# Kernel tuning notes

Measured on AMD Instinct MI355X. Metric: run time of the kernel, lower is better.

Reference implementation:

```python
import jax, jax.numpy as jnp
import numpy as np

B, N, D, H = 4, 2048, 256, 4
DH = D // H
LN_EPS = 1e-5


def setup_inputs() -> dict:
    key = jax.random.key(0)
    ks = jax.random.split(key, 8)
    x = jax.random.normal(ks[0], (B, N, D), dtype=jnp.float32)
    adj = jax.random.randint(ks[1], (N, N), 0, 2, dtype=jnp.int32)
    # parameters (PyTorch Linear stores W as [out, in]; we store [out,in] and apply x @ W.T)
    W = jax.random.normal(ks[2], (D, D), dtype=jnp.float32) * (1.0 / np.sqrt(D))
    a_src = jax.random.normal(ks[3], (H, DH), dtype=jnp.float32)
    a_dst = jax.random.normal(ks[4], (H, DH), dtype=jnp.float32)
    Wo = jax.random.normal(ks[5], (D, D), dtype=jnp.float32) * (1.0 / np.sqrt(D))
    bo = jnp.zeros((D,), dtype=jnp.float32)
    gamma = jnp.ones((D,), dtype=jnp.float32)
    beta = jnp.zeros((D,), dtype=jnp.float32)
    return {"x": x, "adj": adj, "W": W, "a_src": a_src, "a_dst": a_dst,
            "Wo": Wo, "bo": bo, "gamma": gamma, "beta": beta}


def _layer_norm(y, gamma, beta):
    mu = jnp.mean(y, axis=-1, keepdims=True)
    var = jnp.mean((y - mu) ** 2, axis=-1, keepdims=True)
    return (y - mu) * jax.lax.rsqrt(var + LN_EPS) * gamma + beta


def reference(x, adj, W, a_src, a_dst, Wo, bo, gamma, beta):
    # dropout in eval mode (identity)
    b, n, d = x.shape
    h = (x @ W.T).reshape(b, n, H, DH).transpose(0, 2, 1, 3)  # [B,H,N,DH]
    src = jnp.einsum('bhnd,hd->bhn', h, a_src)  # [B,H,N]
    dst = jnp.einsum('bhnd,hd->bhn', h, a_dst)  # [B,H,N]
    e = src[:, :, :, None] + dst[:, :, None, :]  # e[b,h,i,j] = src_i + dst_j
    e = jnp.where(e >= 0, e, 0.2 * e)  # leaky_relu(0.2)
    mask = (adj > 0)[None, None, :, :]
    e = jnp.where(mask, e, -jnp.inf)
    attn = jax.nn.softmax(e, axis=-1)  # [B,H,N,N]
    out = jnp.einsum('bhij,bhjd->bhid', attn, h)  # [B,H,N,DH]
    out = out.transpose(0, 2, 1, 3).reshape(b, n, d)
    out = out @ Wo.T + bo
    return _layer_norm(x + out, gamma, beta)
```

## Files before the change

### kernel.cpp

```cpp
#include <hip/hip_runtime.h>
#include <stdint.h>

#define NTOK 2048
#define DMODEL 256
#define NHEAD 4

typedef __attribute__((ext_vector_type(8))) short short8;
typedef __attribute__((ext_vector_type(4))) float f32x4;

#define MFMA16(a, b, c) __builtin_amdgcn_mfma_f32_16x16x32_bf16(a, b, c, 0, 0, 0)

#if __has_builtin(__builtin_amdgcn_exp2f)
#define EXP2(x) __builtin_amdgcn_exp2f(x)
#else
#define EXP2(x) __expf((x) * 0.6931471805599453f)
#endif

__device__ __forceinline__ unsigned short f2bf(float f) {
  union { float f; unsigned int u; } v; v.f = f;
  unsigned int r = v.u + 0x7FFFu + ((v.u >> 16) & 1u);
  return (unsigned short)(r >> 16);
}

__device__ __forceinline__ f32x4 zero4() {
  f32x4 v; v[0] = 0.f; v[1] = 0.f; v[2] = 0.f; v[3] = 0.f; return v;
}

__global__ void k_prep_pack(const float* __restrict__ x, const float* __restrict__ W,
                            const float* __restrict__ Wo, const int* __restrict__ adj,
                            unsigned short* __restrict__ xbf, unsigned short* __restrict__ Wbf,
                            unsigned short* __restrict__ Wobf,
                            unsigned long long* __restrict__ bits) {
  const int b = blockIdx.x;
  if (b < 2176) {
    int e = (b * 256 + threadIdx.x) * 4;
    const float* s; unsigned short* d; int off;
    if (e < 2097152)              { s = x;  d = xbf;  off = e; }
    else if (e < 2097152 + 65536) { s = W;  d = Wbf;  off = e - 2097152; }
    else                          { s = Wo; d = Wobf; off = e - 2162688; }
    float4 v = *(const float4*)(s + off);
    ushort4 o;
    o.x = f2bf(v.x); o.y = f2bf(v.y); o.z = f2bf(v.z); o.w = f2bf(v.w);
    *(ushort4*)(d + off) = o;
  } else {
    int g = (b - 2176) * 256 + threadIdx.x;
    int v = adj[g];
    unsigned long long m = __ballot(v > 0);
    if ((threadIdx.x & 63) == 0) bits[g >> 6] = m;
  }
}

__global__ void k_gemm1(const unsigned short* __restrict__ xbf, const unsigned short* __restrict__ Wbf,
                        const float* __restrict__ a_src, const float* __restrict__ a_dst,
                        unsigned short* __restrict__ hTg, float* __restrict__ srcv,
                        float* __restrict__ dstv) {
  __shared__ float tile[64][65];
  __shared__ float reds[2][4][64];
  const int tid = threadIdx.x, lane = tid & 63, w = tid >> 6;
  const int g0 = blockIdx.x * 64;
  const int hh = blockIdx.y;
  const int n0 = hh * 64;
  const int l15 = lane & 15, kl = (lane >> 4) * 8;

  const unsigned short* arow = xbf + (size_t)(g0 + w * 16 + l15) * 256 + kl;
  const unsigned short* brow = Wbf + (size_t)(n0 + l15) * 256 + kl;

  f32x4 acc[4];
#pragma unroll
  for (int nf = 0; nf < 4; ++nf) acc[nf] = zero4();

#pragma unroll
  for (int k = 0; k < 256; k += 32) {
    short8 a = *(const short8*)(arow + k);
#pragma unroll
    for (int nf = 0; nf < 4; ++nf) {
      short8 b = *(const short8*)(brow + nf * 4096 + k);
      acc[nf] = MFMA16(a, b, acc[nf]);
    }
  }

  const int rbase = w * 16 + (lane >> 4) * 4;
#pragma unroll
  for (int nf = 0; nf < 4; ++nf)
#pragma unroll
    for (int r = 0; r < 4; ++r)
      tile[rbase + r][nf * 16 + l15] = acc[nf][r];
  __syncthreads();

  const int bh = (g0 >> 11) * NHEAD + hh;
  {
    const int dh = tid >> 2, nq = (tid & 3) * 16;
    const int c = ((g0 & 2047) + nq) >> 5;
    const int k0 = (nq & 16) >> 3;
    unsigned short* dp = hTg + (size_t)bh * 131072 + c * 2048 + dh * 32 + k0 * 8;
    short8 v0, v1;
#pragma unroll
    for (int q = 0; q < 8; ++q) v0[q] = (short)f2bf(tile[nq + q][dh]);
#pragma unroll
    for (int q = 0; q < 8; ++q) v1[q] = (short)f2bf(tile[nq + 8 + q][dh]);
    *(short8*)dp = v0;
    *(short8*)(dp + 8) = v1;
  }
  {
    const int n_loc = tid & 63, q4 = tid >> 6;
    const float* as = a_src + hh * 64 + q4 * 16;
    const float* ad = a_dst + hh * 64 + q4 * 16;
    float ps = 0.f, pd = 0.f;
#pragma unroll
    for (int d2 = 0; d2 < 16; ++d2) {
      float hv = tile[n_loc][q4 * 16 + d2];
      ps += hv * as[d2];
      pd += hv * ad[d2];
    }
    reds[0][q4][n_loc] = ps;
    reds[1][q4][n_loc] = pd;
  }
  __syncthreads();
  if (tid < 64) {
    float s = reds[0][0][tid] + reds[0][1][tid] + reds[0][2][tid] + reds[0][3][tid];
    float d = reds[1][0][tid] + reds[1][1][tid] + reds[1][2][tid] + reds[1][3][tid];
    srcv[(size_t)bh * 2048 + (g0 & 2047) + tid] = s;
    dstv[(size_t)bh * 2048 + (g0 & 2047) + tid] = d;
  }
}

__global__ __launch_bounds__(512, 4) void k_attn(
    const unsigned short* __restrict__ hTg, const float* __restrict__ srcv,
    const float* __restrict__ dstv, const unsigned long long* __restrict__ bits,
    unsigned short* __restrict__ attb) {
  __shared__ float bB_s[2048];
  __shared__ float dD_s[2048];
  __shared__ unsigned long long adjw[64][33];
  __shared__ float src_s[64];
  __shared__ float red[8];
  __shared__ float comb[2][64][40];

  const int tid = threadIdx.x, lane = tid & 63, w = tid >> 6;
  const int orig = blockIdx.x;
  const int lid = (orig & 7) * 64 + (orig >> 3);
  const int bh = lid >> 5;
  const int i0 = (lid & 31) * 64;
  const int rg = w & 1, js = w >> 1;
  const float LOG2E = 1.4426950408889634f;

  float lmax = -3.0e38f;
  {
    const float* dsrc = dstv + (size_t)bh * 2048;
    int idx = tid * 4;
    float4 v = *(const float4*)(dsrc + idx);
    v.x *= LOG2E; v.y *= LOG2E; v.z *= LOG2E; v.w *= LOG2E;
    lmax = fmaxf(fmaxf(v.x, v.y), fmaxf(v.z, v.w));
    float4 Bv, Dv;
    Bv.x = EXP2(v.x); Bv.y = EXP2(v.y); Bv.z = EXP2(v.z); Bv.w = EXP2(v.w);
    Dv.x = EXP2(0.2f * v.x); Dv.y = EXP2(0.2f * v.y);
    Dv.z = EXP2(0.2f * v.z); Dv.w = EXP2(0.2f * v.w);
    *(float4*)(bB_s + idx) = Bv;
    *(float4*)(dD_s + idx) = Dv;
#pragma unroll
    for (int off = 32; off >= 1; off >>= 1) lmax = fmaxf(lmax, __shfl_xor(lmax, off));
    if (lane == 0) red[w] = lmax;
    if (tid < 64) src_s[tid] = srcv[(size_t)bh * 2048 + i0 + tid] * LOG2E;
#pragma unroll
    for (int t = 0; t < 4; ++t) {
      int q = tid + t * 512;
      adjw[q >> 5][q & 31] = bits[(size_t)(i0 + (q >> 5)) * 32 + (q & 31)];
    }
  }
  __syncthreads();
  const float dmax = fmaxf(fmaxf(fmaxf(red[0], red[1]), fmaxf(red[2], red[3])),
                           fmaxf(fmaxf(red[4], red[5]), fmaxf(red[6], red[7])));

  const int l15 = lane & 15, klg = lane >> 4, kl = klg * 8;
  const float src0 = src_s[rg * 32 + l15];
  const float src1 = src_s[rg * 32 + 16 + l15];
  const float sa0 = src0 + dmax, sa1 = src1 + dmax;
  const float m0 = fmaxf(sa0, 0.2f * sa0);
  const float m1 = fmaxf(sa1, 0.2f * sa1);
  const float A0 = EXP2(src0 - m0), C0 = EXP2(fmaf(0.2f, src0, -m0));
  const float A1 = EXP2(src1 - m1), C1 = EXP2(fmaf(0.2f, src1, -m1));
  const float thB0 = EXP2(fminf(fmaxf(-src0, -125.f), 125.f));
  const float thB1 = EXP2(fminf(fmaxf(-src1, -125.f), 125.f));
  const int il0 = rg * 32 + l15, il1 = il0 + 16;
  const int wsel = js >> 1, wsh = (js & 1) * 32 + kl;

  const unsigned short* hgb = hTg + (size_t)bh * 131072;
  const int fragoff = l15 * 32 + klg * 8;

  short8 ones;
#pragma unroll
  for (int q = 0; q < 8; ++q) ones[q] = (short)0x3F80;

  f32x4 acc[2][4], accs[2];
#pragma unroll
  for (int rh = 0; rh < 2; ++rh) {
    accs[rh] = zero4();
#pragma unroll
    for (int nf = 0; nf < 4; ++nf) acc[rh][nf] = zero4();
  }

  short8 pA0, pA1, pA2, pA3, pB0, pB1, pB2, pB3;
  {
    const unsigned short* kp = hgb + js * 2048 + fragoff;
    pA0 = *(const short8*)(kp);
    pA1 = *(const short8*)(kp + 512);
    pA2 = *(const short8*)(kp + 1024);
    pA3 = *(const short8*)(kp + 1536);
  }

#define GAT_TILE(T, C0_, C1_, C2_, C3_, N0_, N1_, N2_, N3_)                       \
  {                                                                               \
    if ((T) < 15) {                                                               \
      const unsigned short* kp = hgb + (((T) + 1) * 4 + js) * 2048 + fragoff;     \
      N0_ = *(const short8*)(kp);                                                 \
      N1_ = *(const short8*)(kp + 512);                                           \
      N2_ = *(const short8*)(kp + 1024);                                          \
      N3_ = *(const short8*)(kp + 1536);                                          \
    }                                                                             \
    const int jo = (T) * 128 + js * 32 + kl;                                      \
    float4 b0 = *(const float4*)(bB_s + jo);                                      \
    float4 b1 = *(const float4*)(bB_s + jo + 4);                                  \
    float4 e0 = *(const float4*)(dD_s + jo);                                      \
    float4 e1 = *(const float4*)(dD_s + jo + 4);                                  \
    float bv[8] = {b0.x, b0.y, b0.z, b0.w, b1.x, b1.y, b1.z, b1.w};               \
    float dq[8] = {e0.x, e0.y, e0.z, e0.w, e1.x, e1.y, e1.z, e1.w};               \
    const unsigned long long w0_ = adjw[il0][2 * (T) + wsel];                     \
    const unsigned long long w1_ = adjw[il1][2 * (T) + wsel];                     \
    {                                                                             \
      const unsigned int byte = (unsigned int)(w0_ >> wsh) & 0xFFu;               \
      float p[8];                                                                 \
      _Pragma("unroll") for (int t8 = 0; t8 < 8; ++t8) {                          \
        const bool pos = bv[t8] >= thB0;                                          \
        const float pv = (pos ? A0 : C0) * (pos ? bv[t8] : dq[t8]);               \
        p[t8] = ((byte >> t8) & 1u) ? pv : 0.f;                                   \
      }                                                                           \
      union { short8 s8; unsigned int u32[4]; } af;                               \
      _Pragma("unroll") for (int q = 0; q < 4; ++q)                               \
        asm("v_cvt_pk_bf16_f32 %0, %1, %2"                                       \
            : "=v"(af.u32[q]) : "v"(p[2 * q]), "v"(p[2 * q + 1]));                \
      accs[0] = MFMA16(af.s8, ones, accs[0]);                                     \
      acc[0][0] = MFMA16(af.s8, C0_, acc[0][0]);                                  \
      acc[0][1] = MFMA16(af.s8, C1_, acc[0][1]);                                  \
      acc[0][2] = MFMA16(af.s8, C2_, acc[0][2]);                                  \
      acc[0][3] = MFMA16(af.s8, C3_, acc[0][3]);                                  \
    }                                                                             \
    {                                                                             \
      const unsigned int byte = (unsigned int)(w1_ >> wsh) & 0xFFu;               \
      float p[8];                                                                 \
      _Pragma("unroll") for (int t8 = 0; t8 < 8; ++t8) {                          \
        const bool pos = bv[t8] >= thB1;                                          \
        const float pv = (pos ? A1 : C1) * (pos ? bv[t8] : dq[t8]);               \
        p[t8] = ((byte >> t8) & 1u) ? pv : 0.f;                                   \
      }                                                                           \
      union { short8 s8; unsigned int u32[4]; } af;                               \
      _Pragma("unroll") for (int q = 0; q < 4; ++q)                               \
        asm("v_cvt_pk_bf16_f32 %0, %1, %2"                                       \
            : "=v"(af.u32[q]) : "v"(p[2 * q]), "v"(p[2 * q + 1]));                \
      accs[1] = MFMA16(af.s8, ones, accs[1]);                                     \
      acc[1][0] = MFMA16(af.s8, C0_, acc[1][0]);                                  \
      acc[1][1] = MFMA16(af.s8, C1_, acc[1][1]);                                  \
      acc[1][2] = MFMA16(af.s8, C2_, acc[1][2]);                                  \
      acc[1][3] = MFMA16(af.s8, C3_, acc[1][3]);                                  \
    }                                                                             \
  }

#pragma unroll 1
  for (int tt = 0; tt < 16; tt += 2) {
    GAT_TILE(tt, pA0, pA1, pA2, pA3, pB0, pB1, pB2, pB3);
    GAT_TILE(tt + 1, pB0, pB1, pB2, pB3, pA0, pA1, pA2, pA3);
  }
#undef GAT_TILE

#pragma unroll 1
  for (int s = 1; s < 4; ++s) {
    if (js == s) {
#pragma unroll
      for (int rh = 0; rh < 2; ++rh) {
#pragma unroll
        for (int nf = 0; nf < 4; ++nf)
#pragma unroll
          for (int r = 0; r < 4; ++r) comb[rg][lane][rh * 20 + nf * 4 + r] = acc[rh][nf][r];
#pragma unroll
        for (int r = 0; r < 4; ++r) comb[rg][lane][rh * 20 + 16 + r] = accs[rh][r];
      }
    }
    __syncthreads();
    if (js == 0) {
#pragma unroll
      for (int rh = 0; rh < 2; ++rh) {
#pragma unroll
        for (int nf = 0; nf < 4; ++nf)
#pragma unroll
          for (int r = 0; r < 4; ++r) acc[rh][nf][r] += comb[rg][lane][rh * 20 + nf * 4 + r];
#pragma unroll
        for (int r = 0; r < 4; ++r) accs[rh][r] += comb[rg][lane][rh * 20 + 16 + r];
      }
    }
    __syncthreads();
  }

  if (js == 0) {
    const int rb = klg * 4;
    const int b = bh >> 2, hh2 = bh & 3;
#pragma unroll
    for (int rh = 0; rh < 2; ++rh) {
      float linv[4];
#pragma unroll
      for (int r = 0; r < 4; ++r) linv[r] = 1.f / accs[rh][r];
#pragma unroll
      for (int nf = 0; nf < 4; ++nf)
#pragma unroll
        for (int r = 0; r < 4; ++r) {
          int i = i0 + rg * 32 + rh * 16 + rb + r;
          size_t o = ((size_t)(b * 2048 + i)) * 256 + hh2 * 64 + nf * 16 + l15;
          attb[o] = f2bf(acc[rh][nf][r] * linv[r]);
        }
    }
  }
}

__global__ void k_gemm2(const unsigned short* __restrict__ attb, const unsigned short* __restrict__ Wobf,
                        const float* __restrict__ bo, const float* __restrict__ x,
                        const float* __restrict__ gamma, const float* __restrict__ beta,
                        float* __restrict__ out) {
  __shared__ float tile[32][260];
  const int tid = threadIdx.x, lane = tid & 63, w = tid >> 6;
  const int g0 = blockIdx.x * 32;
  const int l15 = lane & 15, kl = (lane >> 4) * 8;
  const int rw = (w & 1) * 16;
  const int cb = (w >> 1) * 128;

  const unsigned short* arow = attb + (size_t)(g0 + rw + l15) * 256 + kl;
  const unsigned short* brow = Wobf + (size_t)(cb + l15) * 256 + kl;

  f32x4 acc[8];
#pragma unroll
  for (int nf = 0; nf < 8; ++nf) acc[nf] = zero4();

#pragma unroll
  for (int k = 0; k < 256; k += 32) {
    short8 a = *(const short8*)(arow + k);
#pragma unroll
    for (int nf = 0; nf < 8; ++nf) {
      short8 b = *(const short8*)(brow + (size_t)nf * 4096 + k);
      acc[nf] = MFMA16(a, b, acc[nf]);
    }
  }

  const int rb = rw + (lane >> 4) * 4;
#pragma unroll
  for (int nf = 0; nf < 8; ++nf)
#pragma unroll
    for (int r = 0; r < 4; ++r) {
      int c = cb + nf * 16 + l15;
      tile[rb + r][c] = acc[nf][r] + bo[c];
    }
  __syncthreads();

  const float4 gv = *(const float4*)(gamma + lane * 4);
  const float4 bv = *(const float4*)(beta + lane * 4);
  for (int r = 0; r < 8; ++r) {
    const int gl = w * 8 + r;
    const size_t g = g0 + gl;
    float4 xv = *(const float4*)(x + g * 256 + lane * 4);
    float4 tv = *(float4*)(&tile[gl][lane * 4]);
    float v0 = tv.x + xv.x, v1 = tv.y + xv.y, v2 = tv.z + xv.z, v3 = tv.w + xv.w;
    float sum = v0 + v1 + v2 + v3;
    float sq = v0 * v0 + v1 * v1 + v2 * v2 + v3 * v3;
#pragma unroll
    for (int off = 32; off >= 1; off >>= 1) {
      sum += __shfl_xor(sum, off);
      sq += __shfl_xor(sq, off);
    }
    const float mu = sum * (1.f / 256.f);
    const float var = sq * (1.f / 256.f) - mu * mu;
    const float rs = rsqrtf(var + 1e-5f);
    float4 o;
    o.x = (v0 - mu) * rs * gv.x + bv.x;
    o.y = (v1 - mu) * rs * gv.y + bv.y;
    o.z = (v2 - mu) * rs * gv.z + bv.z;
    o.w = (v3 - mu) * rs * gv.w + bv.w;
    *(float4*)(out + g * 256 + lane * 4) = o;
  }
}

extern "C" void kernel_launch(void* const* d_in, const int* in_sizes, int n_in,
                              void* d_out, int out_size, void* d_ws, size_t ws_size,
                              hipStream_t stream) {
  const float* x      = (const float*)d_in[0];
  const int*   adj    = (const int*)d_in[1];
  const float* W      = (const float*)d_in[2];
  const float* a_src  = (const float*)d_in[3];
  const float* a_dst  = (const float*)d_in[4];
  const float* Wo     = (const float*)d_in[5];
  const float* bo     = (const float*)d_in[6];
  const float* gamma  = (const float*)d_in[7];
  const float* beta   = (const float*)d_in[8];
  float* out = (float*)d_out;

  char* ws = (char*)d_ws;
  unsigned short* xbf       = (unsigned short*)(ws);
  unsigned short* hTg       = (unsigned short*)(ws + (4u << 20));
  unsigned short* attb      = (unsigned short*)(ws + (8u << 20));
  unsigned long long* bits  = (unsigned long long*)(ws + (12u << 20));
  unsigned short* Wbf       = (unsigned short*)(ws + (12u << 20) + (512u << 10));
  unsigned short* Wobf      = (unsigned short*)(ws + (12u << 20) + (640u << 10));
  float* srcv               = (float*)(ws + (12u << 20) + (768u << 10));
  float* dstv               = (float*)(ws + (12u << 20) + (896u << 10));

  k_prep_pack<<<18560, 256, 0, stream>>>(x, W, Wo, adj, xbf, Wbf, Wobf, bits);
  k_gemm1<<<dim3(128, 4), 256, 0, stream>>>(xbf, Wbf, a_src, a_dst, hTg, srcv, dstv);
  k_attn<<<512, 512, 0, stream>>>(hTg, srcv, dstv, bits, attb);
  k_gemm2<<<256, 256, 0, stream>>>(attb, Wobf, bo, x, gamma, beta, out);
}
```

Before: 60.92 us.

## Move adjacency bit-packing into GEMM1 launch and simplify leaky-relu exp selection

The adjacency ballot packing moves out of the prep kernel and into extra blocks of the GEMM1 kernel, so it runs alongside the projection GEMM and the prep kernel only does bf16 conversion. Each extra block now packs four words per thread. In the attention inner loop, the threshold compare and select per element become a max of the two exponential branches. This is valid because exp is monotonic and leaky-relu takes the max of its two linear pieces. Risks are load imbalance inside the combined launch and slight numeric differences from the max formulation.

```diff
diff --git a/kernel.cpp b/kernel.cpp
--- a/kernel.cpp
+++ b/kernel.cpp
@@ -26,39 +26,43 @@
   f32x4 v; v[0] = 0.f; v[1] = 0.f; v[2] = 0.f; v[3] = 0.f; return v;
 }
 
-__global__ void k_prep_pack(const float* __restrict__ x, const float* __restrict__ W,
-                            const float* __restrict__ Wo, const int* __restrict__ adj,
-                            unsigned short* __restrict__ xbf, unsigned short* __restrict__ Wbf,
-                            unsigned short* __restrict__ Wobf,
-                            unsigned long long* __restrict__ bits) {
-  const int b = blockIdx.x;
-  if (b < 2176) {
-    int e = (b * 256 + threadIdx.x) * 4;
-    const float* s; unsigned short* d; int off;
-    if (e < 2097152)              { s = x;  d = xbf;  off = e; }
-    else if (e < 2097152 + 65536) { s = W;  d = Wbf;  off = e - 2097152; }
-    else                          { s = Wo; d = Wobf; off = e - 2162688; }
-    float4 v = *(const float4*)(s + off);
-    ushort4 o;
-    o.x = f2bf(v.x); o.y = f2bf(v.y); o.z = f2bf(v.z); o.w = f2bf(v.w);
-    *(ushort4*)(d + off) = o;
-  } else {
-    int g = (b - 2176) * 256 + threadIdx.x;
-    int v = adj[g];
-    unsigned long long m = __ballot(v > 0);
-    if ((threadIdx.x & 63) == 0) bits[g >> 6] = m;
-  }
-}
-
-__global__ void k_gemm1(const unsigned short* __restrict__ xbf, const unsigned short* __restrict__ Wbf,
-                        const float* __restrict__ a_src, const float* __restrict__ a_dst,
-                        unsigned short* __restrict__ hTg, float* __restrict__ srcv,
-                        float* __restrict__ dstv) {
+__global__ void k_prep(const float* __restrict__ x, const float* __restrict__ W,
+                       const float* __restrict__ Wo,
+                       unsigned short* __restrict__ xbf, unsigned short* __restrict__ Wbf,
+                       unsigned short* __restrict__ Wobf) {
+  int e = (blockIdx.x * 256 + threadIdx.x) * 4;
+  const float* s; unsigned short* d; int off;
+  if (e < 2097152)              { s = x;  d = xbf;  off = e; }
+  else if (e < 2097152 + 65536) { s = W;  d = Wbf;  off = e - 2097152; }
+  else                          { s = Wo; d = Wobf; off = e - 2162688; }
+  float4 v = *(const float4*)(s + off);
+  ushort4 o;
+  o.x = f2bf(v.x); o.y = f2bf(v.y); o.z = f2bf(v.z); o.w = f2bf(v.w);
+  *(ushort4*)(d + off) = o;
+}
+
+__global__ __launch_bounds__(256) void k_g1p(
+    const unsigned short* __restrict__ xbf, const unsigned short* __restrict__ Wbf,
+    const float* __restrict__ a_src, const float* __restrict__ a_dst,
+    const int* __restrict__ adj,
+    unsigned short* __restrict__ hTg, float* __restrict__ srcv, float* __restrict__ dstv,
+    unsigned long long* __restrict__ bits) {
   __shared__ float tile[64][65];
   __shared__ float reds[2][4][64];
+  const int b = blockIdx.x;
+  if (b >= 512) {
+    const int base = (b - 512) * 1024 + threadIdx.x;
+#pragma unroll
+    for (int r = 0; r < 4; ++r) {
+      int g = base + r * 256;
+      unsigned long long m = __ballot(adj[g] > 0);
+      if ((threadIdx.x & 63) == 0) bits[g >> 6] = m;
+    }
+    return;
+  }
   const int tid = threadIdx.x, lane = tid & 63, w = tid >> 6;
-  const int g0 = blockIdx.x * 64;
-  const int hh = blockIdx.y;
+  const int g0 = (b & 127) * 64;
+  const int hh = b >> 7;
   const int n0 = hh * 64;
   const int l15 = lane & 15, kl = (lane >> 4) * 8;
 
@@ -74,8 +78,8 @@
     short8 a = *(const short8*)(arow + k);
 #pragma unroll
     for (int nf = 0; nf < 4; ++nf) {
-      short8 b = *(const short8*)(brow + nf * 4096 + k);
-      acc[nf] = MFMA16(a, b, acc[nf]);
+      short8 bb = *(const short8*)(brow + nf * 4096 + k);
+      acc[nf] = MFMA16(a, bb, acc[nf]);
     }
   }
 
@@ -178,8 +182,6 @@
   const float m1 = fmaxf(sa1, 0.2f * sa1);
   const float A0 = EXP2(src0 - m0), C0 = EXP2(fmaf(0.2f, src0, -m0));
   const float A1 = EXP2(src1 - m1), C1 = EXP2(fmaf(0.2f, src1, -m1));
-  const float thB0 = EXP2(fminf(fmaxf(-src0, -125.f), 125.f));
-  const float thB1 = EXP2(fminf(fmaxf(-src1, -125.f), 125.f));
   const int il0 = rg * 32 + l15, il1 = il0 + 16;
   const int wsel = js >> 1, wsh = (js & 1) * 32 + kl;
 
@@ -229,8 +231,7 @@
       const unsigned int byte = (unsigned int)(w0_ >> wsh) & 0xFFu;               \
       float p[8];                                                                 \
       _Pragma("unroll") for (int t8 = 0; t8 < 8; ++t8) {                          \
-        const bool pos = bv[t8] >= thB0;                                          \
-        const float pv = (pos ? A0 : C0) * (pos ? bv[t8] : dq[t8]);               \
+        const float pv = fmaxf(A0 * bv[t8], C0 * dq[t8]);                         \
         p[t8] = ((byte >> t8) & 1u) ? pv : 0.f;                                   \
       }                                                                           \
       union { short8 s8; unsigned int u32[4]; } af;                               \
@@ -247,8 +248,7 @@
       const unsigned int byte = (unsigned int)(w1_ >> wsh) & 0xFFu;               \
       float p[8];                                                                 \
       _Pragma("unroll") for (int t8 = 0; t8 < 8; ++t8) {                          \
-        const bool pos = bv[t8] >= thB1;                                          \
-        const float pv = (pos ? A1 : C1) * (pos ? bv[t8] : dq[t8]);               \
+        const float pv = fmaxf(A1 * bv[t8], C1 * dq[t8]);                         \
         p[t8] = ((byte >> t8) & 1u) ? pv : 0.f;                                   \
       }                                                                           \
       union { short8 s8; unsigned int u32[4]; } af;                               \
@@ -407,8 +407,8 @@
   float* srcv               = (float*)(ws + (12u << 20) + (768u << 10));
   float* dstv               = (float*)(ws + (12u << 20) + (896u << 10));
 
-  k_prep_pack<<<18560, 256, 0, stream>>>(x, W, Wo, adj, xbf, Wbf, Wobf, bits);
-  k_gemm1<<<dim3(128, 4), 256, 0, stream>>>(xbf, Wbf, a_src, a_dst, hTg, srcv, dstv);
+  k_prep<<<2176, 256, 0, stream>>>(x, W, Wo, xbf, Wbf, Wobf);
+  k_g1p<<<4608, 256, 0, stream>>>(xbf, Wbf, a_src, a_dst, adj, hTg, srcv, dstv, bits);
   k_attn<<<512, 512, 0, stream>>>(hTg, srcv, dstv, bits, attb);
   k_gemm2<<<256, 256, 0, stream>>>(attb, Wobf, bo, x, gamma, beta, out);
 }
```

New measurement: 60.63 us, median of 2. No clear change (-0.5%).
